# Kernel tuning notes

Measured on AMD Instinct MI355X. Metric: run time of the kernel, lower is better.

The kernel has to match this reference:

```python
import jax, jax.numpy as jnp
import numpy as np
from jax import lax

TOP_K = 2

def _unfold(x_img, k):
    # F.unfold(kernel=k, stride=k): [B,C,H,W] -> [B, C*k*k, L], column index c*k*k + kh*k + kw
    B, C, H, W = x_img.shape
    Hp, Wp = H // k, W // k
    u = x_img.reshape(B, C, Hp, k, Wp, k).transpose(0, 1, 3, 5, 2, 4)
    return u.reshape(B, C * k * k, Hp * Wp)

def _fold(p, k, H, W):
    # F.fold inverse of non-overlapping unfold: [B, C*k*k, L] -> [B,C,H,W]
    B = p.shape[0]
    C = p.shape[1] // (k * k)
    Hp, Wp = H // k, W // k
    u = p.reshape(B, C, k, k, Hp, Wp).transpose(0, 1, 4, 2, 5, 3)
    return u.reshape(B, C, H, W)

def setup_inputs() -> dict:
    key = jax.random.key(0)
    ks = jax.random.split(key, 6)
    B, H, W, C, F, E, P = 8, 64, 64, 384, 1536, 8, 4
    N = H * W
    x = jax.random.normal(ks[0], (B, N, C), dtype=jnp.float32)
    gate_w = jax.random.normal(ks[1], (E, C, P, P), dtype=jnp.float32) * 0.01
    w1 = jax.random.normal(ks[2], (E, C, F), dtype=jnp.float32) * (1.0 / np.sqrt(C))
    b1 = jax.random.normal(ks[3], (E, F), dtype=jnp.float32) * 0.01
    w2 = jax.random.normal(ks[4], (E, F, C), dtype=jnp.float32) * (1.0 / np.sqrt(F))
    b2 = jax.random.normal(ks[5], (E, C), dtype=jnp.float32) * 0.01
    return {"x": x, "gate_w": gate_w, "w1": w1, "b1": b1, "w2": w2, "b2": b2, "H": H, "W": W}

def reference(x, gate_w, w1, b1, w2, b2, H, W):
    B, N, C = x.shape
    E, _, P, _ = gate_w.shape
    k2 = P * P
    Hp, Wp = H // P, W // P
    L = Hp * Wp
    x_img = jnp.transpose(x, (0, 2, 1)).reshape(B, C, H, W)
    # router: strided conv -> logits per patch
    logits_map = lax.conv_general_dilated(
        x_img, gate_w, window_strides=(P, P), padding='VALID',
        dimension_numbers=('NCHW', 'OIHW', 'NCHW'))  # [B,E,Hp,Wp]
    router_logits = jnp.transpose(logits_map, (0, 2, 3, 1)).reshape(B, L, E)
    probs = jax.nn.softmax(router_logits, axis=-1)
    ew, ei = lax.top_k(probs, TOP_K)  # [B,L,topk]
    ew = ew / (jnp.sum(ew, axis=-1, keepdims=True) + 1e-9)
    # expand to token level (faithful to original's reshape/flatten ordering)
    ei_tok = jnp.broadcast_to(ei[:, :, None, :], (B, L, k2, TOP_K)).reshape(-1, TOP_K)
    ew_tok = jnp.broadcast_to(ew[:, :, None, :], (B, L, k2, TOP_K)).reshape(-1, TOP_K)
    # unfold + the original's (scrambled) reshape(B, C, L, k2)
    U = _unfold(x_img, P)  # [B, C*k2, L]
    x_patches = jnp.transpose(U.reshape(B, C, L, k2), (0, 2, 3, 1))  # [B,L,k2,C]
    flat_x = x_patches.reshape(-1, C)  # [T,C], T = B*L*k2
    # combine weights: zero for experts not in top-k == masked dispatch math
    cw = jnp.zeros((flat_x.shape[0], E), dtype=flat_x.dtype)
    for kk in range(TOP_K):
        cw = cw + jax.nn.one_hot(ei_tok[:, kk], E, dtype=flat_x.dtype) * ew_tok[:, kk:kk + 1]
    out = jnp.zeros_like(flat_x)
    for e in range(E):
        h = jax.nn.gelu(flat_x @ w1[e] + b1[e], approximate=False)
        y = h @ w2[e] + b2[e]
        out = out + cw[:, e:e + 1] * y
    # fold back (mirrors original's reshape/permute exactly)
    o = jnp.transpose(out.reshape(B, L, k2, C), (0, 3, 1, 2)).reshape(B, C * k2, L)
    out_img = _fold(o, P, H, W)  # [B,C,H,W]
    # original: output.transpose(1,2).reshape(B,N,C) on NCHW tensor
    output = jnp.transpose(out_img, (0, 2, 1, 3)).reshape(B, N, C)
    return output
```

## Files before the change

kernel.cpp:

```cpp
#include <hip/hip_runtime.h>
#include <hip/hip_bf16.h>

#define BB   8
#define HH   64
#define WWID 64
#define CC   384
#define FF   1536
#define EE   8
#define LL   256
#define MTOTMAX 66560
#define NTMAX   520

typedef unsigned short ushort_t;
typedef __attribute__((ext_vector_type(4))) unsigned short u16x4;
typedef __attribute__((ext_vector_type(8))) short          s16x8;
typedef __attribute__((ext_vector_type(4))) float          f32x4;

__device__ __forceinline__ float bf2f(ushort_t u) {
  union { unsigned int i; float f; } v; v.i = ((unsigned int)u) << 16; return v.f;
}
__device__ __forceinline__ ushort_t f2bf(float f) {
  union { float f; unsigned int i; } v; v.f = f;
  unsigned int u = v.i;
  u += 0x7fffu + ((u >> 16) & 1u);
  return (ushort_t)(u >> 16);
}
__device__ __forceinline__ float gelu_f(float x) {
  float u  = 0.70710678118654752f * x;
  float au = fabsf(u);
  float t  = 1.0f / (1.0f + 0.3275911f * au);
  float poly = t * (0.254829592f + t * (-0.284496736f + t * (1.421413741f +
               t * (-1.453152027f + t * 1.061405429f))));
  float ea = 1.0f - poly * __expf(-au * au);
  float erfv = (x < 0.f) ? -ea : ea;
  return 0.5f * x * (1.0f + erfv);
}

#define GLDS(g, l) __builtin_amdgcn_global_load_lds( \
    (const __attribute__((address_space(1))) void*)(g), \
    (__attribute__((address_space(3))) void*)(l), 16, 0, 0)

__global__ __launch_bounds__(256) void k_transpose(const float* __restrict__ src,
                                                   ushort_t* __restrict__ dst,
                                                   int R, int Cd) {
  __shared__ ushort_t tile[32][33];
  int e  = blockIdx.z;
  int c0 = blockIdx.x * 32, r0 = blockIdx.y * 32;
  int tx = threadIdx.x & 31, ty = threadIdx.x >> 5;
  const float* s = src + (size_t)e * R * Cd;
  ushort_t*    d = dst + (size_t)e * R * Cd;
  #pragma unroll
  for (int i = 0; i < 32; i += 8)
    tile[ty + i][tx] = f2bf(s[(size_t)(r0 + ty + i) * Cd + c0 + tx]);
  __syncthreads();
  #pragma unroll
  for (int i = 0; i < 32; i += 8)
    d[(size_t)(c0 + ty + i) * R + r0 + tx] = tile[tx][ty + i];
}

__global__ void k_tgw(const float* __restrict__ gw, float* __restrict__ gwt) {
  int e = blockIdx.x, t = threadIdx.x;
  for (int i = t; i < CC * 16; i += 256) {
    int c = i >> 4, p = i & 15;
    gwt[((size_t)e * 16 + p) * CC + c] = gw[(size_t)e * CC * 16 + i];
  }
}

__global__ __launch_bounds__(256) void k_router(const float* __restrict__ x,
                                                const float* __restrict__ gwt,
                                                int* __restrict__ re, float* __restrict__ rw,
                                                int* __restrict__ cnt) {
  int bid = blockIdx.x;
  int b = bid >> 8, l2 = bid & 255;
  int hp = l2 >> 4, wp = l2 & 15;
  int t = threadIdx.x;
  int e = t >> 5, lane = t & 31;
  const float* xb = x + (size_t)b * (HH * WWID) * CC;
  const float* ge = gwt + (size_t)e * 16 * CC;
  float acc = 0.f;
  #pragma unroll
  for (int p = 0; p < 16; ++p) {
    int pix = (hp * 4 + (p >> 2)) * 64 + wp * 4 + (p & 3);
    const float* xr = xb + (size_t)pix * CC;
    const float* gr = ge + (size_t)p * CC;
    #pragma unroll
    for (int it = 0; it < 3; ++it) {
      f32x4 xv = *reinterpret_cast<const f32x4*>(xr + it * 128 + lane * 4);
      f32x4 gv = *reinterpret_cast<const f32x4*>(gr + it * 128 + lane * 4);
      acc += xv.x * gv.x + xv.y * gv.y + xv.z * gv.z + xv.w * gv.w;
    }
  }
  #pragma unroll
  for (int d = 16; d; d >>= 1) acc += __shfl_down(acc, d, 32);
  __shared__ float logits[EE];
  if (lane == 0) logits[e] = acc;
  __syncthreads();
  if (t == 0) {
    float m = logits[0];
    #pragma unroll
    for (int i = 1; i < EE; ++i) m = fmaxf(m, logits[i]);
    float p[EE]; float s = 0.f;
    #pragma unroll
    for (int i = 0; i < EE; ++i) { p[i] = __expf(logits[i] - m); s += p[i]; }
    #pragma unroll
    for (int i = 0; i < EE; ++i) p[i] /= s;
    int e0 = 0;
    #pragma unroll
    for (int i = 1; i < EE; ++i) if (p[i] > p[e0]) e0 = i;
    int e1 = (e0 == 0) ? 1 : 0;
    #pragma unroll
    for (int i = 0; i < EE; ++i) if (i != e0 && p[i] > p[e1]) e1 = i;
    float s2 = p[e0] + p[e1] + 1e-9f;
    re[bid * 2 + 0] = e0;  re[bid * 2 + 1] = e1;
    rw[bid * 2 + 0] = p[e0] / s2;  rw[bid * 2 + 1] = p[e1] / s2;
    atomicAdd(&cnt[e0], 16);
    atomicAdd(&cnt[e1], 16);
  }
}

__global__ void k_pad(const int* __restrict__ cnt, int* __restrict__ cntp,
                      int* __restrict__ basep, int* __restrict__ tile2e,
                      int* __restrict__ gids, float* __restrict__ gwts) {
  __shared__ int s_cnt[EE], s_cntp[EE], s_base[EE + 1];
  int t = threadIdx.x;
  if (t == 0) {
    int b = 0;
    for (int e = 0; e < EE; ++e) {
      int c  = cnt[e];
      int cp = (c + 127) & ~127;
      s_cnt[e] = c; s_cntp[e] = cp; s_base[e] = b;
      b += cp;
    }
    s_base[EE] = b;
  }
  __syncthreads();
  if (t < EE) { cntp[t] = s_cntp[t]; basep[t] = s_base[t]; }
  if (t == EE) basep[EE] = s_base[EE];
  int ntot = s_base[EE] >> 7;
  for (int g = t; g < ntot; g += 256) {
    int e = 0;
    #pragma unroll
    for (int i = 1; i < EE; ++i) if (g * 128 >= s_base[i]) e = i;
    tile2e[g] = e;
  }
  for (int e = 0; e < EE; ++e)
    for (int i = s_cnt[e] + t; i < s_cntp[e]; i += 256) {
      gids[s_base[e] + i] = -1;
      gwts[s_base[e] + i] = 0.f;
    }
}

__global__ void k_assign(const int* __restrict__ re, const float* __restrict__ rw,
                         const int* __restrict__ basep, int* __restrict__ cnt2,
                         int* __restrict__ gids, float* __restrict__ gwts,
                         int* __restrict__ inv) {
  int i = blockIdx.x * blockDim.x + threadIdx.x;
  if (i >= BB * LL * 2) return;
  int pat = i >> 1, slot = i & 1;
  int b = pat >> 8, l2 = pat & 255;
  int e = re[i];
  float w = rw[i];
  int t2 = l2 >> 4, hp = l2 & 15;
  int kh = t2 >> 2, kw = t2 & 3;
  int h = hp * 4 + kh;
  int row = basep[e] + atomicAdd(&cnt2[e], 16);
  #pragma unroll
  for (int j = 0; j < 16; ++j) {
    int wpix = j * 4 + kw;
    int pix = (b << 12) + (h << 6) + wpix;
    gids[row + j] = pix;
    gwts[row + j] = w;
    inv[(slot << 15) + pix] = row + j;
  }
}

__global__ __launch_bounds__(256) void k_gather(const float* __restrict__ x,
                                                const int* __restrict__ gids,
                                                const int* __restrict__ basep,
                                                ushort_t* __restrict__ Xc, int t0) {
  int g = t0 + blockIdx.x;
  if (g * 128 >= basep[EE]) return;
  __shared__ int s_id[128];
  int t = threadIdx.x;
  if (t < 128) s_id[t] = gids[g * 128 + t];
  __syncthreads();
  ushort_t* dst = Xc + (size_t)blockIdx.x * 128 * CC;
  for (int i = t; i < 128 * 96; i += 256) {
    int row = i / 96, ch = (i % 96) * 4;
    int id = s_id[row];
    f32x4 v = (f32x4){0.f, 0.f, 0.f, 0.f};
    if (id >= 0) v = *reinterpret_cast<const f32x4*>(x + (size_t)(id & 32767) * CC + ch);
    u16x4 o = {f2bf(v.x), f2bf(v.y), f2bf(v.z), f2bf(v.w)};
    *reinterpret_cast<u16x4*>(dst + (size_t)row * CC + ch) = o;
  }
}

__global__ __launch_bounds__(256, 3) void k_gemm1(const ushort_t* __restrict__ Xc,
                                                  const ushort_t* __restrict__ w1t,
                                                  const float* __restrict__ b1,
                                                  const int* __restrict__ basep,
                                                  const int* __restrict__ tile2e,
                                                  ushort_t* __restrict__ Hc, int t0) {
  int g = t0 + blockIdx.y;
  if (g * 128 >= basep[EE]) return;
  int e = tile2e[g], fg = blockIdx.x;
  __shared__ ushort_t As[12 * 512];
  __shared__ ushort_t Bs[8 * 512];
  int t = threadIdx.x, w = t >> 6, lane = t & 63;
  int l15 = lane & 15, q = lane >> 4;
  const ushort_t* a_src = w1t + ((size_t)e * FF + fg * 192) * CC;
  const ushort_t* b_src = Xc + (size_t)blockIdx.y * 128 * CC;
  f32x4 acc[6][4];
  #pragma unroll
  for (int i = 0; i < 6; ++i)
    #pragma unroll
    for (int j = 0; j < 4; ++j) acc[i][j] = (f32x4){0.f, 0.f, 0.f, 0.f};

  for (int k0 = 0; k0 < CC; k0 += 32) {
    __syncthreads();
    #pragma unroll
    for (int c = 0; c < 5; ++c) {
      int ch = w * 5 + c;
      if (ch < 12) GLDS(a_src + (size_t)(ch * 16 + l15) * CC + k0 + q * 8, As + ch * 512);
      else         GLDS(b_src + (size_t)((ch - 12) * 16 + l15) * CC + k0 + q * 8, Bs + (ch - 12) * 512);
    }
    __syncthreads();
    s16x8 af[6], bf[4];
    #pragma unroll
    for (int i = 0; i < 6; ++i)
      af[i] = *reinterpret_cast<const s16x8*>(As + ((w & 1) * 6 + i) * 512 + lane * 8);
    #pragma unroll
    for (int j = 0; j < 4; ++j)
      bf[j] = *reinterpret_cast<const s16x8*>(Bs + ((w >> 1) * 4 + j) * 512 + lane * 8);
    #pragma unroll
    for (int i = 0; i < 6; ++i)
      #pragma unroll
      for (int j = 0; j < 4; ++j)
        acc[i][j] = __builtin_amdgcn_mfma_f32_16x16x32_bf16(af[i], bf[j], acc[i][j], 0, 0, 0);
  }

  ushort_t* hbase = Hc + (size_t)blockIdx.y * 128 * FF;
  int fb = fg * 192 + (w & 1) * 96 + q * 4;
  f32x4 bias[6];
  #pragma unroll
  for (int i = 0; i < 6; ++i)
    bias[i] = *reinterpret_cast<const f32x4*>(b1 + (size_t)e * FF + fb + i * 16);
  #pragma unroll
  for (int j = 0; j < 4; ++j) {
    int m = (w >> 1) * 64 + j * 16 + l15;
    ushort_t* hp = hbase + (size_t)m * FF + fb;
    #pragma unroll
    for (int i = 0; i < 6; ++i) {
      u16x4 v;
      #pragma unroll
      for (int r = 0; r < 4; ++r)
        v[r] = f2bf(gelu_f(acc[i][j][r] + bias[i][r]));
      *reinterpret_cast<u16x4*>(hp + i * 16) = v;
    }
  }
}

__global__ __launch_bounds__(256, 3) void k_gemm2(const ushort_t* __restrict__ Hc,
                                                  const ushort_t* __restrict__ w2t,
                                                  const float* __restrict__ b2,
                                                  const int* __restrict__ basep,
                                                  const int* __restrict__ tile2e,
                                                  const float* __restrict__ gwts,
                                                  ushort_t* __restrict__ y, int t0) {
  int g = t0 + blockIdx.y;
  if (g * 128 >= basep[EE]) return;
  int e = tile2e[g], nb = blockIdx.x;
  __shared__ ushort_t As[12 * 512];
  __shared__ ushort_t Bs[8 * 512];
  __shared__ float s_w[128];
  int t = threadIdx.x, w = t >> 6, lane = t & 63;
  int l15 = lane & 15, q = lane >> 4;
  if (t < 128) s_w[t] = gwts[g * 128 + t];
  const ushort_t* a_src = w2t + ((size_t)e * CC + nb * 192) * FF;
  const ushort_t* b_src = Hc + (size_t)blockIdx.y * 128 * FF;
  f32x4 acc[6][4];
  #pragma unroll
  for (int i = 0; i < 6; ++i)
    #pragma unroll
    for (int j = 0; j < 4; ++j) acc[i][j] = (f32x4){0.f, 0.f, 0.f, 0.f};

  for (int k0 = 0; k0 < FF; k0 += 32) {
    __syncthreads();
    #pragma unroll
    for (int c = 0; c < 5; ++c) {
      int ch = w * 5 + c;
      if (ch < 12) GLDS(a_src + (size_t)(ch * 16 + l15) * FF + k0 + q * 8, As + ch * 512);
      else         GLDS(b_src + (size_t)((ch - 12) * 16 + l15) * FF + k0 + q * 8, Bs + (ch - 12) * 512);
    }
    __syncthreads();
    s16x8 af[6], bf[4];
    #pragma unroll
    for (int i = 0; i < 6; ++i)
      af[i] = *reinterpret_cast<const s16x8*>(As + ((w & 1) * 6 + i) * 512 + lane * 8);
    #pragma unroll
    for (int j = 0; j < 4; ++j)
      bf[j] = *reinterpret_cast<const s16x8*>(Bs + ((w >> 1) * 4 + j) * 512 + lane * 8);
    #pragma unroll
    for (int i = 0; i < 6; ++i)
      #pragma unroll
      for (int j = 0; j < 4; ++j)
        acc[i][j] = __builtin_amdgcn_mfma_f32_16x16x32_bf16(af[i], bf[j], acc[i][j], 0, 0, 0);
  }

  int cb = nb * 192 + (w & 1) * 96 + q * 4;
  f32x4 bias[6];
  #pragma unroll
  for (int i = 0; i < 6; ++i)
    bias[i] = *reinterpret_cast<const f32x4*>(b2 + (size_t)e * CC + cb + i * 16);
  ushort_t* ybase = y + (size_t)g * 128 * CC;
  #pragma unroll
  for (int j = 0; j < 4; ++j) {
    int m = (w >> 1) * 64 + j * 16 + l15;
    float wt = s_w[m];
    ushort_t* yp = ybase + (size_t)m * CC + cb;
    #pragma unroll
    for (int i = 0; i < 6; ++i) {
      u16x4 v;
      #pragma unroll
      for (int r = 0; r < 4; ++r)
        v[r] = f2bf((acc[i][j][r] + bias[i][r]) * wt);
      *reinterpret_cast<u16x4*>(yp + i * 16) = v;
    }
  }
}

__global__ __launch_bounds__(256) void k_final(const ushort_t* __restrict__ y,
                                               const int* __restrict__ inv,
                                               float* __restrict__ out) {
  int bid = blockIdx.x;
  __shared__ float tile[64][193];
  __shared__ int s_r0[64], s_r1[64];
  int t = threadIdx.x;
  if (t < 64) {
    s_r0[t] = inv[(bid << 6) + t];
    s_r1[t] = inv[32768 + (bid << 6) + t];
  }
  __syncthreads();
  float* dst = out + (size_t)bid * CC * WWID;
  #pragma unroll
  for (int half = 0; half < 2; ++half) {
    int c0 = half * 192;
    for (int i = t; i < 64 * 48; i += 256) {
      int w = i / 48, c4 = (i % 48) * 4;
      u16x4 a = *reinterpret_cast<const u16x4*>(y + (size_t)s_r0[w] * CC + c0 + c4);
      u16x4 b = *reinterpret_cast<const u16x4*>(y + (size_t)s_r1[w] * CC + c0 + c4);
      #pragma unroll
      for (int k = 0; k < 4; ++k)
        tile[w][c4 + k] = bf2f(a[k]) + bf2f(b[k]);
    }
    __syncthreads();
    for (int i = t; i < 64 * 192; i += 256) {
      int cl = i / 64, w = i % 64;
      dst[(size_t)(c0 + cl) * WWID + w] = tile[w][cl];
    }
    __syncthreads();
  }
}

extern "C" void kernel_launch(void* const* d_in, const int* in_sizes, int n_in,
                              void* d_out, int out_size, void* d_ws, size_t ws_size,
                              hipStream_t stream) {
  const float* x  = (const float*)d_in[0];
  const float* gw = (const float*)d_in[1];
  const float* w1 = (const float*)d_in[2];
  const float* b1 = (const float*)d_in[3];
  const float* w2 = (const float*)d_in[4];
  const float* b2 = (const float*)d_in[5];

  const size_t fixed = (size_t)EE * FF * CC * 2 * 2
                     + (size_t)MTOTMAX * CC * 2
                     + (size_t)EE * 16 * CC * 4
                     + (size_t)MTOTMAX * 4 * 2
                     + (size_t)65536 * 4
                     + (size_t)BB * LL * 2 * 4 * 2
                     + (size_t)NTMAX * 4
                     + 1024;
  const int cands[6] = {32768, 16384, 8192, 4096, 2048, 1024};
  int MC = 1024;
  for (int i = 0; i < 6; ++i)
    if (fixed + (size_t)cands[i] * 3840 <= ws_size) { MC = cands[i]; break; }
  const int npass = (MTOTMAX + MC - 1) / MC;
  const int ntile = MC / 128;

  char* ws = (char*)d_ws;
  size_t off = 0;
  ushort_t* Xc   = (ushort_t*)(ws + off); off += (size_t)MC * CC * 2;
  ushort_t* Hc   = (ushort_t*)(ws + off); off += (size_t)MC * FF * 2;
  ushort_t* w1t  = (ushort_t*)(ws + off); off += (size_t)EE * FF * CC * 2;
  ushort_t* w2t  = (ushort_t*)(ws + off); off += (size_t)EE * FF * CC * 2;
  ushort_t* y    = (ushort_t*)(ws + off); off += (size_t)MTOTMAX * CC * 2;
  float* gwt   = (float*)(ws + off); off += (size_t)EE * 16 * CC * 4;
  int*   gids  = (int*)(ws + off);   off += (size_t)MTOTMAX * 4;
  float* gwts  = (float*)(ws + off); off += (size_t)MTOTMAX * 4;
  int*   inv   = (int*)(ws + off);   off += (size_t)65536 * 4;
  int*   re    = (int*)(ws + off);   off += (size_t)BB * LL * 2 * 4;
  float* rw    = (float*)(ws + off); off += (size_t)BB * LL * 2 * 4;
  int*   tile2e= (int*)(ws + off);   off += (size_t)NTMAX * 4;
  int*   cnt   = (int*)(ws + off);   off += 64;
  int*   cnt2  = (int*)(ws + off);   off += 64;
  int*   cntp  = (int*)(ws + off);   off += 64;
  int*   basep = (int*)(ws + off);   off += 64;

  hipMemsetAsync(cnt, 0, 128, stream);

  k_transpose<<<dim3(FF / 32, CC / 32, EE), 256, 0, stream>>>(w1, w1t, CC, FF);
  k_transpose<<<dim3(CC / 32, FF / 32, EE), 256, 0, stream>>>(w2, w2t, FF, CC);
  k_tgw<<<EE, 256, 0, stream>>>(gw, gwt);
  k_router<<<BB * LL, 256, 0, stream>>>(x, gwt, re, rw, cnt);
  k_pad<<<1, 256, 0, stream>>>(cnt, cntp, basep, tile2e, gids, gwts);
  k_assign<<<16, 256, 0, stream>>>(re, rw, basep, cnt2, gids, gwts, inv);

  for (int p = 0; p < npass; ++p) {
    int t0 = p * ntile;
    k_gather<<<ntile, 256, 0, stream>>>(x, gids, basep, Xc, t0);
    k_gemm1<<<dim3(FF / 192, ntile), 256, 0, stream>>>(Xc, w1t, b1, basep, tile2e, Hc, t0);
    k_gemm2<<<dim3(CC / 192, ntile), 256, 0, stream>>>(Hc, w2t, b2, basep, tile2e, gwts, y, t0);
  }
  k_final<<<BB * HH, 256, 0, stream>>>(y, inv, (float*)d_out);
}
```

Measured before the change: 698.2 us.

## Double-buffer LDS in expert GEMMs, remap blocks per XCD, enlarge pass chunk

Both expert GEMM kernels now double-buffer their LDS tiles, so the next K-slice's global-to-LDS load is issued while the current slice feeds the MFMAs, and one barrier per iteration is dropped. Blocks are launched on a 1D grid and remapped so that all column blocks of the same token tile land on the same XCD, which is meant to improve L2 reuse of the activation tile. The chunk-size candidates are enlarged so that, when the workspace allows it, fewer passes are needed. The trade-off is double the LDS per block, which may lower occupancy, and larger intermediate buffers.

After: 777.3 us. 11.3% more time.

```diff
diff --git a/kernel.cpp b/kernel.cpp
--- a/kernel.cpp
+++ b/kernel.cpp
@@ -200,38 +200,54 @@
                                                   const float* __restrict__ b1,
                                                   const int* __restrict__ basep,
                                                   const int* __restrict__ tile2e,
-                                                  ushort_t* __restrict__ Hc, int t0) {
-  int g = t0 + blockIdx.y;
+                                                  ushort_t* __restrict__ Hc,
+                                                  int t0, int ntp) {
+  int n = blockIdx.x;
+  int xcd = n & 7, lc = n >> 3;
+  int tl = lc >> 3, fg = lc & 7;
+  int tloc = xcd + 8 * tl;
+  if (tloc >= ntp) return;
+  int g = t0 + tloc;
   if (g * 128 >= basep[EE]) return;
-  int e = tile2e[g], fg = blockIdx.x;
-  __shared__ ushort_t As[12 * 512];
-  __shared__ ushort_t Bs[8 * 512];
+  int e = tile2e[g];
+  __shared__ ushort_t As[2][12 * 512];
+  __shared__ ushort_t Bs[2][8 * 512];
   int t = threadIdx.x, w = t >> 6, lane = t & 63;
   int l15 = lane & 15, q = lane >> 4;
   const ushort_t* a_src = w1t + ((size_t)e * FF + fg * 192) * CC;
-  const ushort_t* b_src = Xc + (size_t)blockIdx.y * 128 * CC;
+  const ushort_t* b_src = Xc + (size_t)tloc * 128 * CC;
   f32x4 acc[6][4];
   #pragma unroll
   for (int i = 0; i < 6; ++i)
     #pragma unroll
     for (int j = 0; j < 4; ++j) acc[i][j] = (f32x4){0.f, 0.f, 0.f, 0.f};
 
-  for (int k0 = 0; k0 < CC; k0 += 32) {
+  #pragma unroll
+  for (int c = 0; c < 5; ++c) {
+    int ch = w * 5 + c;
+    if (ch < 12) GLDS(a_src + (size_t)(ch * 16 + l15) * CC + q * 8, &As[0][ch * 512]);
+    else         GLDS(b_src + (size_t)((ch - 12) * 16 + l15) * CC + q * 8, &Bs[0][(ch - 12) * 512]);
+  }
+
+  for (int it = 0; it < 12; ++it) {
+    int cur = it & 1;
     __syncthreads();
-    #pragma unroll
-    for (int c = 0; c < 5; ++c) {
-      int ch = w * 5 + c;
-      if (ch < 12) GLDS(a_src + (size_t)(ch * 16 + l15) * CC + k0 + q * 8, As + ch * 512);
-      else         GLDS(b_src + (size_t)((ch - 12) * 16 + l15) * CC + k0 + q * 8, Bs + (ch - 12) * 512);
-    }
-    __syncthreads();
+    if (it + 1 < 12) {
+      int k0 = (it + 1) * 32;
+      #pragma unroll
+      for (int c = 0; c < 5; ++c) {
+        int ch = w * 5 + c;
+        if (ch < 12) GLDS(a_src + (size_t)(ch * 16 + l15) * CC + k0 + q * 8, &As[cur ^ 1][ch * 512]);
+        else         GLDS(b_src + (size_t)((ch - 12) * 16 + l15) * CC + k0 + q * 8, &Bs[cur ^ 1][(ch - 12) * 512]);
+      }
+    }
     s16x8 af[6], bf[4];
     #pragma unroll
     for (int i = 0; i < 6; ++i)
-      af[i] = *reinterpret_cast<const s16x8*>(As + ((w & 1) * 6 + i) * 512 + lane * 8);
+      af[i] = *reinterpret_cast<const s16x8*>(&As[cur][((w & 1) * 6 + i) * 512 + lane * 8]);
     #pragma unroll
     for (int j = 0; j < 4; ++j)
-      bf[j] = *reinterpret_cast<const s16x8*>(Bs + ((w >> 1) * 4 + j) * 512 + lane * 8);
+      bf[j] = *reinterpret_cast<const s16x8*>(&Bs[cur][((w >> 1) * 4 + j) * 512 + lane * 8]);
     #pragma unroll
     for (int i = 0; i < 6; ++i)
       #pragma unroll
@@ -239,7 +255,7 @@
         acc[i][j] = __builtin_amdgcn_mfma_f32_16x16x32_bf16(af[i], bf[j], acc[i][j], 0, 0, 0);
   }
 
-  ushort_t* hbase = Hc + (size_t)blockIdx.y * 128 * FF;
+  ushort_t* hbase = Hc + (size_t)tloc * 128 * FF;
   int fb = fg * 192 + (w & 1) * 96 + q * 4;
   f32x4 bias[6];
   #pragma unroll
@@ -266,40 +282,56 @@
                                                   const int* __restrict__ basep,
                                                   const int* __restrict__ tile2e,
                                                   const float* __restrict__ gwts,
-                                                  ushort_t* __restrict__ y, int t0) {
-  int g = t0 + blockIdx.y;
+                                                  ushort_t* __restrict__ y,
+                                                  int t0, int ntp) {
+  int n = blockIdx.x;
+  int xcd = n & 7, lc = n >> 3;
+  int tl = lc >> 1, nb = lc & 1;
+  int tloc = xcd + 8 * tl;
+  if (tloc >= ntp) return;
+  int g = t0 + tloc;
   if (g * 128 >= basep[EE]) return;
-  int e = tile2e[g], nb = blockIdx.x;
-  __shared__ ushort_t As[12 * 512];
-  __shared__ ushort_t Bs[8 * 512];
+  int e = tile2e[g];
+  __shared__ ushort_t As[2][12 * 512];
+  __shared__ ushort_t Bs[2][8 * 512];
   __shared__ float s_w[128];
   int t = threadIdx.x, w = t >> 6, lane = t & 63;
   int l15 = lane & 15, q = lane >> 4;
   if (t < 128) s_w[t] = gwts[g * 128 + t];
   const ushort_t* a_src = w2t + ((size_t)e * CC + nb * 192) * FF;
-  const ushort_t* b_src = Hc + (size_t)blockIdx.y * 128 * FF;
+  const ushort_t* b_src = Hc + (size_t)tloc * 128 * FF;
   f32x4 acc[6][4];
   #pragma unroll
   for (int i = 0; i < 6; ++i)
     #pragma unroll
     for (int j = 0; j < 4; ++j) acc[i][j] = (f32x4){0.f, 0.f, 0.f, 0.f};
 
-  for (int k0 = 0; k0 < FF; k0 += 32) {
+  #pragma unroll
+  for (int c = 0; c < 5; ++c) {
+    int ch = w * 5 + c;
+    if (ch < 12) GLDS(a_src + (size_t)(ch * 16 + l15) * FF + q * 8, &As[0][ch * 512]);
+    else         GLDS(b_src + (size_t)((ch - 12) * 16 + l15) * FF + q * 8, &Bs[0][(ch - 12) * 512]);
+  }
+
+  for (int it = 0; it < 48; ++it) {
+    int cur = it & 1;
     __syncthreads();
-    #pragma unroll
-    for (int c = 0; c < 5; ++c) {
-      int ch = w * 5 + c;
-      if (ch < 12) GLDS(a_src + (size_t)(ch * 16 + l15) * FF + k0 + q * 8, As + ch * 512);
-      else         GLDS(b_src + (size_t)((ch - 12) * 16 + l15) * FF + k0 + q * 8, Bs + (ch - 12) * 512);
-    }
-    __syncthreads();
+    if (it + 1 < 48) {
+      int k0 = (it + 1) * 32;
+      #pragma unroll
+      for (int c = 0; c < 5; ++c) {
+        int ch = w * 5 + c;
+        if (ch < 12) GLDS(a_src + (size_t)(ch * 16 + l15) * FF + k0 + q * 8, &As[cur ^ 1][ch * 512]);
+        else         GLDS(b_src + (size_t)((ch - 12) * 16 + l15) * FF + k0 + q * 8, &Bs[cur ^ 1][(ch - 12) * 512]);
+      }
+    }
     s16x8 af[6], bf[4];
     #pragma unroll
     for (int i = 0; i < 6; ++i)
-      af[i] = *reinterpret_cast<const s16x8*>(As + ((w & 1) * 6 + i) * 512 + lane * 8);
+      af[i] = *reinterpret_cast<const s16x8*>(&As[cur][((w & 1) * 6 + i) * 512 + lane * 8]);
     #pragma unroll
     for (int j = 0; j < 4; ++j)
-      bf[j] = *reinterpret_cast<const s16x8*>(Bs + ((w >> 1) * 4 + j) * 512 + lane * 8);
+      bf[j] = *reinterpret_cast<const s16x8*>(&Bs[cur][((w >> 1) * 4 + j) * 512 + lane * 8]);
     #pragma unroll
     for (int i = 0; i < 6; ++i)
       #pragma unroll
@@ -380,12 +412,13 @@
                      + (size_t)BB * LL * 2 * 4 * 2
                      + (size_t)NTMAX * 4
                      + 1024;
-  const int cands[6] = {32768, 16384, 8192, 4096, 2048, 1024};
+  const int cands[7] = {66560, 33280, 16640, 8320, 4096, 2048, 1024};
   int MC = 1024;
-  for (int i = 0; i < 6; ++i)
+  for (int i = 0; i < 7; ++i)
     if (fixed + (size_t)cands[i] * 3840 <= ws_size) { MC = cands[i]; break; }
   const int npass = (MTOTMAX + MC - 1) / MC;
   const int ntile = MC / 128;
+  const int nt8   = (ntile + 7) & ~7;
 
   char* ws = (char*)d_ws;
   size_t off = 0;
@@ -418,8 +451,8 @@
   for (int p = 0; p < npass; ++p) {
     int t0 = p * ntile;
     k_gather<<<ntile, 256, 0, stream>>>(x, gids, basep, Xc, t0);
-    k_gemm1<<<dim3(FF / 192, ntile), 256, 0, stream>>>(Xc, w1t, b1, basep, tile2e, Hc, t0);
-    k_gemm2<<<dim3(CC / 192, ntile), 256, 0, stream>>>(Hc, w2t, b2, basep, tile2e, gwts, y, t0);
+    k_gemm1<<<nt8 * 8, 256, 0, stream>>>(Xc, w1t, b1, basep, tile2e, Hc, t0, ntile);
+    k_gemm2<<<nt8 * 2, 256, 0, stream>>>(Hc, w2t, b2, basep, tile2e, gwts, y, t0, ntile);
   }
   k_final<<<BB * HH, 256, 0, stream>>>(y, inv, (float*)d_out);
 }
```
